# Kernel tuning notes

Hardware: AMD Instinct MI355X
Metric: run time of the kernel (lower is better)

## Reference

```python
import jax, jax.numpy as jnp
import numpy as np

K = 9          # neighbors
DIL = 1        # dilation
BN_EPS = 1e-5

def _bn(x, g, b, m, v):
    # inference batchnorm over channel (last) dim
    return (x - m) * (g * jax.lax.rsqrt(v + BN_EPS)) + b

def setup_inputs() -> dict:
    key = jax.random.key(0)
    ks = jax.random.split(key, 4)
    B, C, H, W = 8, 192, 56, 56
    Ch = 384
    s = 0.02
    return {
        'x': jax.random.normal(ks[0], (B, C, H, W), jnp.float32),
        'fc1_w': jax.random.normal(ks[1], (C, C), jnp.float32) * s,
        'fc1_b': jnp.zeros((C,), jnp.float32),
        'bn1_g': jnp.ones((C,), jnp.float32), 'bn1_b': jnp.zeros((C,), jnp.float32),
        'bn1_m': jnp.zeros((C,), jnp.float32), 'bn1_v': jnp.ones((C,), jnp.float32),
        'gc_w': jax.random.normal(ks[2], (Ch, 2 * C), jnp.float32) * s,
        'gc_b': jnp.zeros((Ch,), jnp.float32),
        'bn2_g': jnp.ones((Ch,), jnp.float32), 'bn2_b': jnp.zeros((Ch,), jnp.float32),
        'bn2_m': jnp.zeros((Ch,), jnp.float32), 'bn2_v': jnp.ones((Ch,), jnp.float32),
        'fc2_w': jax.random.normal(ks[3], (C, Ch), jnp.float32) * s,
        'fc2_b': jnp.zeros((C,), jnp.float32),
        'bn3_g': jnp.ones((C,), jnp.float32), 'bn3_b': jnp.zeros((C,), jnp.float32),
        'bn3_m': jnp.zeros((C,), jnp.float32), 'bn3_v': jnp.ones((C,), jnp.float32),
    }

def reference(x, fc1_w, fc1_b, bn1_g, bn1_b, bn1_m, bn1_v,
              gc_w, gc_b, bn2_g, bn2_b, bn2_m, bn2_v,
              fc2_w, fc2_b, bn3_g, bn3_b, bn3_m, bn3_v):
    B, C, H, W = x.shape
    N = H * W
    xf = x.reshape(B, C, N).transpose(0, 2, 1)          # (B, N, C) nodes
    shortcut = xf
    # fc1: 1x1 conv + BN
    h = _bn(jnp.einsum('bnc,oc->bno', xf, fc1_w) + fc1_b, bn1_g, bn1_b, bn1_m, bn1_v)
    # dynamic KNN on L2-normalized features (ViG dense_knn_matrix)
    hn = h / jnp.maximum(jnp.linalg.norm(h, axis=-1, keepdims=True), 1e-12)
    sim = jnp.einsum('bnc,bmc->bnm', hn, hn)            # (B, N, N) cosine sim
    _, idx = jax.lax.top_k(sim, K * DIL)                # nearest (incl. self)
    idx = idx[..., ::DIL]                               # dilated neighbors (B,N,K)
    # gather neighbor features
    x_j = jax.vmap(lambda hb, ib: hb[ib])(h, idx)       # (B, N, K, C)
    x_i = h[:, :, None, :]                              # (B, N, 1, C)
    feat = jnp.concatenate([jnp.broadcast_to(x_i, x_j.shape), x_j - x_i], axis=-1)
    # EdgeConv: conv then max over neighbors
    e = jnp.einsum('bnke,oe->bnko', feat, gc_w) + gc_b  # (B, N, K, Ch)
    m = jnp.max(e, axis=2)                              # (B, N, Ch)
    m = jax.nn.gelu(_bn(m, bn2_g, bn2_b, bn2_m, bn2_v), approximate=False)
    # fc2: 1x1 conv + BN, residual
    out = _bn(jnp.einsum('bnh,oh->bno', m, fc2_w) + fc2_b, bn3_g, bn3_b, bn3_m, bn3_v)
    out = out + shortcut
    return out.transpose(0, 2, 1).reshape(B, C, H, W)
```

## Files before the change

kernel.cpp:

```cpp
#include <hip/hip_runtime.h>

#define BDIM 256
#define NB 8
#define NC 192
#define NN 3136
#define NCH 384
#define NK 9
#define NROW (NB * NN)

typedef __attribute__((ext_vector_type(8))) short short8;
typedef __attribute__((ext_vector_type(4))) float f32x4;

__device__ __forceinline__ unsigned short f2bf(float f) {
  union { float f; unsigned u; } x{f};
  unsigned r = x.u + 0x7fff + ((x.u >> 16) & 1);
  return (unsigned short)(r >> 16);
}

__device__ __forceinline__ float bf2f(unsigned u16) {
  union { unsigned u; float f; } x{u16 << 16};
  return x.f;
}

__device__ __forceinline__ unsigned umax_(unsigned a, unsigned b) { return a > b ? a : b; }
__device__ __forceinline__ unsigned umin_(unsigned a, unsigned b) { return a < b ? a : b; }
#define UMAX3(a, b, c) umax_(umax_((a), (b)), (c))
#define CXD(x, y)                      \
  {                                    \
    unsigned h_ = umax_(x, y);         \
    unsigned l_ = umin_(x, y);         \
    x = h_;                            \
    y = l_;                            \
  }

__device__ __forceinline__ unsigned simkey(float f, unsigned it) {
  union { float f; unsigned u; } x{f + 2.0f};
  return (x.u & 0xFFFFF000u) | it;
}

__device__ __forceinline__ void gload16(const char* g, char* l) {
  __builtin_amdgcn_global_load_lds(
      (const __attribute__((address_space(1))) unsigned int*)g,
      (__attribute__((address_space(3))) unsigned int*)l, 16, 0, 0);
}

__device__ __forceinline__ void stage_tile(const char* gbase, char* lbuf, int t) {
#pragma unroll
  for (int i = 0; i < 6; ++i) {
    int L = (i * 256 + t) * 16;
    int m = L / 384;
    int kb = L - m * 384;
    gload16(gbase + m * 384 + (kb ^ ((m & 7) << 4)), lbuf + L);
  }
}

__global__ __launch_bounds__(BDIM) void k0_convw(
    const float* __restrict__ gw, const float* __restrict__ f1w,
    const float* __restrict__ f2w, unsigned short* __restrict__ gcwb,
    unsigned short* __restrict__ fc1b, unsigned short* __restrict__ fc2b) {
  int i = (blockIdx.x * BDIM + threadIdx.x) * 4;
  const float* src;
  unsigned short* dst;
  if (i < 147456) {
    int o = i / NC, k = i - o * NC;
    src = gw + (size_t)(o < NCH ? o : o - NCH) * (2 * NC) + (o < NCH ? 0 : NC) + k;
    dst = gcwb + i;
  } else if (i < 184320) {
    int j = i - 147456;
    src = f1w + j;
    dst = fc1b + j;
  } else {
    int j = i - 184320;
    int o = j / NCH, k = j - o * NCH;
    int oc = o >> 6, om = o & 63;
    int kh = k / 192, km = k - kh * 192;
    src = f2w + j;
    dst = fc2b + ((size_t)((oc * 2 + kh) * 64 + om)) * 192 + km;
  }
  float4 v = *(const float4*)src;
  uint2 u;
  u.x = (unsigned)f2bf(v.x) | ((unsigned)f2bf(v.y) << 16);
  u.y = (unsigned)f2bf(v.z) | ((unsigned)f2bf(v.w) << 16);
  *(uint2*)dst = u;
}

__global__ __launch_bounds__(384) void k0b_params(
    const float* __restrict__ f1b, const float* __restrict__ g1,
    const float* __restrict__ b1, const float* __restrict__ m1,
    const float* __restrict__ v1, const float* __restrict__ gcb,
    const float* __restrict__ g2, const float* __restrict__ b2,
    const float* __restrict__ m2, const float* __restrict__ v2,
    const float* __restrict__ f2b, const float* __restrict__ g3,
    const float* __restrict__ b3, const float* __restrict__ m3,
    const float* __restrict__ v3, float* __restrict__ sc1,
    float* __restrict__ sh1, float* __restrict__ sc2, float* __restrict__ sh2,
    float* __restrict__ sc3, float* __restrict__ sh3) {
  int c = threadIdx.x;
  if (c < NC) {
    float s1 = g1[c] * rsqrtf(v1[c] + 1e-5f);
    sc1[c] = s1;
    sh1[c] = (f1b[c] - m1[c]) * s1 + b1[c];
    float s3 = g3[c] * rsqrtf(v3[c] + 1e-5f);
    sc3[c] = s3;
    sh3[c] = (f2b[c] - m3[c]) * s3 + b3[c];
  }
  float s2 = g2[c] * rsqrtf(v2[c] + 1e-5f);
  sc2[c] = s2;
  sh2[c] = (gcb[c] - m2[c]) * s2 + b2[c];
}

__global__ __launch_bounds__(BDIM) void k1_mfma(
    const float* __restrict__ x, const unsigned short* __restrict__ fc1b,
    const float* __restrict__ sc1, const float* __restrict__ sh1,
    unsigned short* __restrict__ hnb, float* __restrict__ normo) {
  __shared__ __align__(16) char abuf[2][24576];
  int t = threadIdx.x;
  int b = blockIdx.x / 49, n0 = (blockIdx.x % 49) * 64;
  int lane = t & 63, w = t >> 6;
  int l15 = lane & 15, l4 = lane >> 4;
  int n = n0 + w * 16 + l15;
  short8 bfr[6];
  {
    const float* xcol = x + (size_t)b * NC * NN + n;
#pragma unroll
    for (int ks = 0; ks < 6; ++ks) {
      union { short8 s; unsigned u[4]; } pk;
#pragma unroll
      for (int j = 0; j < 4; ++j) {
        float v0 = xcol[(size_t)(ks * 32 + l4 * 8 + 2 * j) * NN];
        float v1 = xcol[(size_t)(ks * 32 + l4 * 8 + 2 * j + 1) * NN];
        pk.u[j] = (unsigned)f2bf(v0) | ((unsigned)f2bf(v1) << 16);
      }
      bfr[ks] = pk.s;
    }
  }
  f32x4 acc[3][4];
#pragma unroll
  for (int oc = 0; oc < 3; ++oc)
#pragma unroll
    for (int sub = 0; sub < 4; ++sub) acc[oc][sub] = {0.f, 0.f, 0.f, 0.f};

  const char* wB = (const char*)fc1b;
  stage_tile(wB, abuf[0], t);
  __syncthreads();
  for (int oc = 0; oc < 3; ++oc) {
    int cur = oc & 1;
    if (oc < 2) stage_tile(wB + (size_t)(oc + 1) * 24576, abuf[cur ^ 1], t);
#pragma unroll
    for (int sub = 0; sub < 4; ++sub) {
      int r_ = sub * 16 + l15;
      int rbase = r_ * 384, sw = (r_ & 7) << 4;
#pragma unroll
      for (int ks = 0; ks < 6; ++ks) {
        short8 af = *(const short8*)&abuf[cur][rbase + ((ks * 64 + l4 * 16) ^ sw)];
        acc[oc][sub] = __builtin_amdgcn_mfma_f32_16x16x32_bf16(af, bfr[ks],
                                                               acc[oc][sub], 0, 0, 0);
      }
    }
    __syncthreads();
  }
  float p = 0.f;
#pragma unroll
  for (int oc = 0; oc < 3; ++oc)
#pragma unroll
    for (int sub = 0; sub < 4; ++sub) {
      int c4 = oc * 64 + sub * 16 + l4 * 4;
      float s_[4], h_[4];
      *(float4*)s_ = *(const float4*)&sc1[c4];
      *(float4*)h_ = *(const float4*)&sh1[c4];
#pragma unroll
      for (int r = 0; r < 4; ++r) {
        float v = acc[oc][sub][r] * s_[r] + h_[r];
        acc[oc][sub][r] = v;
        p += v * v;
      }
    }
  p += __shfl_xor(p, 16);
  p += __shfl_xor(p, 32);
  float nr = fmaxf(sqrtf(p), 1e-12f);
  float iv = 1.f / nr;
  if (l4 == 0) normo[(size_t)b * NN + n] = nr;
#pragma unroll
  for (int oc = 0; oc < 3; ++oc)
#pragma unroll
    for (int sub = 0; sub < 4; ++sub) {
      uint2 u;
      u.x = (unsigned)f2bf(acc[oc][sub][0] * iv) |
            ((unsigned)f2bf(acc[oc][sub][1] * iv) << 16);
      u.y = (unsigned)f2bf(acc[oc][sub][2] * iv) |
            ((unsigned)f2bf(acc[oc][sub][3] * iv) << 16);
      *(uint2*)&hnb[(size_t)(b * NN + n) * NC + oc * 64 + sub * 16 + l4 * 4] = u;
    }
}

__global__ __launch_bounds__(512) void k23_fused(
    const unsigned short* __restrict__ hnb, const float* __restrict__ norm,
    const unsigned short* __restrict__ gcwb, unsigned* __restrict__ candK,
    unsigned short* __restrict__ P, unsigned short* __restrict__ Q) {
  __shared__ __align__(16) char abuf[2][12288];
  int t = threadIdx.x;
  int bid = blockIdx.x;
  int b = bid & 7;
  int j = bid >> 3;
  int lane = t & 63, w = t >> 6;
  int l15 = lane & 15, l4 = lane >> 4;
  int wg = w & 3, sub = w >> 2;
  const unsigned short* hb = hnb + (size_t)b * NN * NC;

  int LA = t * 16;
  int mA = LA / 384, kbA = LA - mA * 384;
  int gA = mA * 384 + (kbA ^ ((mA & 7) << 4));
  int LB = (384 + t) * 16;
  int mB = LB / 384, kbB = LB - mB * 384;
  int gB = mB * 384 + (kbB ^ ((mB & 7) << 4));
  bool stg = (t < 384);
  int r_ = sub * 16 + l15;
  int rbase = r_ * 384, sw = (r_ & 7) << 4;
  int dso[6];
#pragma unroll
  for (int ks = 0; ks < 6; ++ks) dso[ks] = rbase + ((ks * 64 + l4 * 16) ^ sw);

  if (j % 5 != 4) {
    int idx2a = (j / 5) * 4 + (j % 5);
    int n0 = (idx2a >> 2) * 64;
    int seg = idx2a & 3;
    int mt0 = (98 * seg) / 4, mt1 = (98 * (seg + 1)) / 4;
    const char* hbB = (const char*)hb;

    short8 bfr[6];
    {
      const short8* brow =
          (const short8*)(hb + (size_t)(n0 + wg * 16 + l15) * NC + l4 * 8);
#pragma unroll
      for (int ks = 0; ks < 6; ++ks) bfr[ks] = brow[ks * 4];
    }
    unsigned tk[NK];
#pragma unroll
    for (int r = 0; r < NK; ++r) tk[r] = 0u;

    {
      const char* src = hbB + (size_t)mt0 * 12288;
      if (stg) { gload16(src + gA, abuf[0] + LA); gload16(src + gB, abuf[0] + LB); }
    }
    __syncthreads();
    int nt = mt1 - mt0;
    for (int ti = 0; ti < nt; ++ti) {
      int cur = ti & 1;
      if (ti + 1 < nt) {
        const char* src = hbB + (size_t)(mt0 + ti + 1) * 12288;
        char* dl = abuf[cur ^ 1];
        if (stg) { gload16(src + gA, dl + LA); gload16(src + gB, dl + LB); }
        asm volatile("s_waitcnt vmcnt(2)" ::: "memory");
      } else {
        asm volatile("s_waitcnt vmcnt(0)" ::: "memory");
      }
      __builtin_amdgcn_s_barrier();
      __builtin_amdgcn_sched_barrier(0);
      const char* lb = abuf[cur];
      short8 af[6];
#pragma unroll
      for (int ks = 0; ks < 6; ++ks) af[ks] = *(const short8*)&lb[dso[ks]];
      f32x4 acc = {0.f, 0.f, 0.f, 0.f};
#pragma unroll
      for (int ks = 0; ks < 6; ++ks)
        acc = __builtin_amdgcn_mfma_f32_16x16x32_bf16(af[ks], bfr[ks], acc, 0, 0, 0);
      unsigned mknd = (unsigned)(4095 - ((mt0 + ti) * 32 + sub * 16 + l4 * 4));
      unsigned c0 = simkey(acc[0], mknd);
      unsigned c1 = simkey(acc[1], mknd - 1);
      unsigned c2 = simkey(acc[2], mknd - 2);
      unsigned c3 = simkey(acc[3], mknd - 3);
      CXD(c0, c1); CXD(c2, c3); CXD(c0, c2); CXD(c1, c3); CXD(c1, c2);
      tk[8] = UMAX3(UMAX3(tk[8], umin_(tk[7], c0), umin_(tk[6], c1)),
                    umin_(tk[5], c2), umin_(tk[4], c3));
      tk[7] = UMAX3(UMAX3(tk[7], umin_(tk[6], c0), umin_(tk[5], c1)),
                    umin_(tk[4], c2), umin_(tk[3], c3));
      tk[6] = UMAX3(UMAX3(tk[6], umin_(tk[5], c0), umin_(tk[4], c1)),
                    umin_(tk[3], c2), umin_(tk[2], c3));
      tk[5] = UMAX3(UMAX3(tk[5], umin_(tk[4], c0), umin_(tk[3], c1)),
                    umin_(tk[2], c2), umin_(tk[1], c3));
      tk[4] = UMAX3(UMAX3(tk[4], umin_(tk[3], c0), umin_(tk[2], c1)),
                    umin_(tk[1], c2), umin_(tk[0], c3));
      tk[3] = UMAX3(UMAX3(tk[3], c3, umin_(tk[2], c0)),
                    umin_(tk[1], c1), umin_(tk[0], c2));
      tk[2] = umax_(UMAX3(tk[2], c2, umin_(tk[1], c0)), umin_(tk[0], c1));
      tk[1] = UMAX3(tk[1], c1, umin_(tk[0], c0));
      tk[0] = umax_(tk[0], c0);
      __builtin_amdgcn_sched_barrier(0);
      __builtin_amdgcn_s_barrier();
    }
    unsigned* mkeys = (unsigned*)&abuf[0][0];
    int rw = wg * 16 + l15;
#pragma unroll
    for (int r = 0; r < NK; ++r) mkeys[(rw * 8 + sub * 4 + l4) * NK + r] = tk[r];
    __syncthreads();
    if (t < 256) {
      int row = t >> 2, g = t & 3;
      unsigned* a = &mkeys[(row * 8 + g) * NK];
      const unsigned* c = &mkeys[(row * 8 + g + 4) * NK];
      unsigned best[NK];
#pragma unroll
      for (int r = 0; r < NK; ++r) best[r] = 0u;
#pragma unroll
      for (int s = 0; s < 2 * NK; ++s) {
        unsigned cur_k = s < NK ? a[s] : c[s - NK];
#pragma unroll
        for (int q = 0; q < NK; ++q) {
          unsigned hi = best[q] > cur_k ? best[q] : cur_k;
          unsigned lo = best[q] > cur_k ? cur_k : best[q];
          best[q] = hi;
          cur_k = lo;
        }
      }
#pragma unroll
      for (int r = 0; r < NK; ++r) a[r] = best[r];
    }
    __syncthreads();
    if (t < 64) {
      const unsigned* src = &mkeys[(t * 8) * NK];
      unsigned best[NK];
#pragma unroll
      for (int r = 0; r < NK; ++r) best[r] = 0u;
      for (int s = 0; s < 36; ++s) {
        unsigned cur_k = src[s];
#pragma unroll
        for (int q = 0; q < NK; ++q) {
          unsigned hi = best[q] > cur_k ? best[q] : cur_k;
          unsigned lo = best[q] > cur_k ? cur_k : best[q];
          best[q] = hi;
          cur_k = lo;
        }
      }
      size_t row = (size_t)b * NN + n0 + t;
#pragma unroll
      for (int r = 0; r < NK; ++r)
        candK[(size_t)(seg * NK + r) * NROW + row] = best[r];
    }
  } else {
    int jj = j / 5;
    int n0 = jj * 64;
    int n = n0 + wg * 16 + l15;
    short8 bfr[6];
    {
      const short8* brow = (const short8*)(hb + (size_t)n * NC + l4 * 8);
#pragma unroll
      for (int ks = 0; ks < 6; ++ks) bfr[ks] = brow[ks * 4];
    }
    float nrm = norm[(size_t)b * NN + n];
    size_t orow = (size_t)b * NN + n;
    const char* wB = (const char*)gcwb;

    if (stg) { gload16(wB + gA, abuf[0] + LA); gload16(wB + gB, abuf[0] + LB); }
    __syncthreads();
    for (int ch = 0; ch < 24; ++ch) {
      int cur = ch & 1;
      if (ch < 23) {
        const char* src = wB + (size_t)(ch + 1) * 12288;
        char* dl = abuf[cur ^ 1];
        if (stg) { gload16(src + gA, dl + LA); gload16(src + gB, dl + LB); }
        asm volatile("s_waitcnt vmcnt(2)" ::: "memory");
      } else {
        asm volatile("s_waitcnt vmcnt(0)" ::: "memory");
      }
      __builtin_amdgcn_s_barrier();
      __builtin_amdgcn_sched_barrier(0);
      const char* lb = abuf[cur];
      f32x4 acc = {0.f, 0.f, 0.f, 0.f};
#pragma unroll
      for (int ks = 0; ks < 6; ++ks) {
        short8 af = *(const short8*)&lb[dso[ks]];
        acc = __builtin_amdgcn_mfma_f32_16x16x32_bf16(af, bfr[ks], acc, 0, 0, 0);
      }
      int o = ch * 32 + sub * 16 + l4 * 4;
      f32x4 st = acc * nrm;
      unsigned short* dst = (o < NCH) ? P : Q;
      int oo = (o < NCH) ? o : o - NCH;
      uint2 u;
      u.x = (unsigned)f2bf(st[0]) | ((unsigned)f2bf(st[1]) << 16);
      u.y = (unsigned)f2bf(st[2]) | ((unsigned)f2bf(st[3]) << 16);
      *(uint2*)&dst[orow * NCH + oo] = u;
      __builtin_amdgcn_sched_barrier(0);
      __builtin_amdgcn_s_barrier();
    }
  }
}

__global__ __launch_bounds__(BDIM) void k2b_merge(const unsigned* __restrict__ candK,
                                                  int* __restrict__ idxo) {
  int row = blockIdx.x * BDIM + threadIdx.x;
  unsigned tk[NK];
#pragma unroll
  for (int r = 0; r < NK; ++r) tk[r] = 0u;
  for (int s = 0; s < 4 * NK; ++s) {
    unsigned cur = candK[(size_t)s * NROW + row];
#pragma unroll
    for (int j = 0; j < NK; ++j) {
      unsigned hi = tk[j] > cur ? tk[j] : cur;
      unsigned lo = tk[j] > cur ? cur : tk[j];
      tk[j] = hi;
      cur = lo;
    }
  }
#pragma unroll
  for (int r = 0; r < NK; ++r)
    idxo[(size_t)row * NK + r] = 4095 - (int)(tk[r] & 4095u);
}

__global__ __launch_bounds__(BDIM) void k4_gathermax(
    const unsigned short* __restrict__ P, const unsigned short* __restrict__ Q,
    const int* __restrict__ idx, const float* __restrict__ sc2,
    const float* __restrict__ sh2, unsigned short* __restrict__ mbh) {
  int t = threadIdx.x;
  int lane = t & 63, wv = t >> 6;
  int b = blockIdx.x & 7;
  int n = (int)(blockIdx.x >> 3) * 4 + wv;
  size_t row = (size_t)b * NN + n;
  const int* ip = idx + row * NK;
  int id[NK];
#pragma unroll
  for (int k = 0; k < NK; ++k) id[k] = ip[k];
  const unsigned short* Qb = Q + (size_t)b * NN * NCH;
  const unsigned short* Pr = P + row * NCH;
  const unsigned short* Qr = Qb + (size_t)n * NCH;
#pragma unroll
  for (int j = 0; j < 3; ++j) {
    int o = j * 128 + lane * 2;
    float mx0 = -1e30f, mx1 = -1e30f;
#pragma unroll
    for (int k = 0; k < NK; ++k) {
      unsigned g = *(const unsigned*)&Qb[(size_t)id[k] * NCH + o];
      mx0 = fmaxf(mx0, bf2f(g & 0xffffu));
      mx1 = fmaxf(mx1, bf2f(g >> 16));
    }
    unsigned pv = *(const unsigned*)&Pr[o];
    unsigned qv = *(const unsigned*)&Qr[o];
    float2 ss = *(const float2*)&sc2[o];
    float2 hh = *(const float2*)&sh2[o];
    float e0 = bf2f(pv & 0xffffu) - bf2f(qv & 0xffffu) + mx0;
    float e1 = bf2f(pv >> 16) - bf2f(qv >> 16) + mx1;
    float y0 = e0 * ss.x + hh.x;
    float y1 = e1 * ss.y + hh.y;
    float ge0 = 0.5f * y0 * (1.f + erff(y0 * 0.70710678118654752f));
    float ge1 = 0.5f * y1 * (1.f + erff(y1 * 0.70710678118654752f));
    *(unsigned*)&mbh[row * NCH + o] =
        (unsigned)f2bf(ge0) | ((unsigned)f2bf(ge1) << 16);
  }
}

__global__ __launch_bounds__(BDIM) void k5_mfma(
    const unsigned short* __restrict__ mbh, const unsigned short* __restrict__ fc2b,
    const float* __restrict__ sc3, const float* __restrict__ sh3,
    const float* __restrict__ x, float* __restrict__ out) {
  __shared__ __align__(16) char abuf[2][24576];
  int t = threadIdx.x;
  int bid = blockIdx.x;
  int b = bid / 147;
  int rem = bid % 147;
  int n0 = (rem / 3) * 64;
  int oc = rem % 3;
  int lane = t & 63, w = t >> 6;
  int l15 = lane & 15, l4 = lane >> 4;
  int n = n0 + w * 16 + l15;
  short8 bfr[12];
  {
    const short8* brow = (const short8*)(mbh + (size_t)(b * NN + n) * NCH + l4 * 8);
#pragma unroll
    for (int kh = 0; kh < 2; ++kh)
#pragma unroll
      for (int ks = 0; ks < 6; ++ks) bfr[kh * 6 + ks] = brow[kh * 24 + ks * 4];
  }
  f32x4 acc[4];
#pragma unroll
  for (int sub = 0; sub < 4; ++sub) acc[sub] = {0.f, 0.f, 0.f, 0.f};

  const char* wt = (const char*)fc2b + (size_t)oc * 2 * 24576;
  stage_tile(wt, abuf[0], t);
  __syncthreads();
  for (int kh = 0; kh < 2; ++kh) {
    if (kh == 0) stage_tile(wt + 24576, abuf[1], t);
#pragma unroll
    for (int sub = 0; sub < 4; ++sub) {
      int r_ = sub * 16 + l15;
      int rbase = r_ * 384, sw = (r_ & 7) << 4;
#pragma unroll
      for (int ks = 0; ks < 6; ++ks) {
        short8 af = *(const short8*)&abuf[kh][rbase + ((ks * 64 + l4 * 16) ^ sw)];
        acc[sub] = __builtin_amdgcn_mfma_f32_16x16x32_bf16(af, bfr[kh * 6 + ks],
                                                           acc[sub], 0, 0, 0);
      }
    }
    __syncthreads();
  }
  const float* xb_ = x + (size_t)b * NC * NN;
  float* ob = out + (size_t)b * NC * NN;
#pragma unroll
  for (int sub = 0; sub < 4; ++sub) {
    int c4 = oc * 64 + sub * 16 + l4 * 4;
    float s_[4], h_[4];
    *(float4*)s_ = *(const float4*)&sc3[c4];
    *(float4*)h_ = *(const float4*)&sh3[c4];
#pragma unroll
    for (int r = 0; r < 4; ++r) {
      size_t off = (size_t)(c4 + r) * NN + n;
      ob[off] = acc[sub][r] * s_[r] + h_[r] + xb_[off];
    }
  }
}

extern "C" void kernel_launch(void* const* d_in, const int* in_sizes, int n_in,
                              void* d_out, int out_size, void* d_ws, size_t ws_size,
                              hipStream_t stream) {
  const float* x = (const float*)d_in[0];
  const float* fc1_w = (const float*)d_in[1];
  const float* fc1_b = (const float*)d_in[2];
  const float* bn1_g = (const float*)d_in[3];
  const float* bn1_b = (const float*)d_in[4];
  const float* bn1_m = (const float*)d_in[5];
  const float* bn1_v = (const float*)d_in[6];
  const float* gc_w = (const float*)d_in[7];
  const float* gc_b = (const float*)d_in[8];
  const float* bn2_g = (const float*)d_in[9];
  const float* bn2_b = (const float*)d_in[10];
  const float* bn2_m = (const float*)d_in[11];
  const float* bn2_v = (const float*)d_in[12];
  const float* fc2_w = (const float*)d_in[13];
  const float* fc2_b = (const float*)d_in[14];
  const float* bn3_g = (const float*)d_in[15];
  const float* bn3_b = (const float*)d_in[16];
  const float* bn3_m = (const float*)d_in[17];
  const float* bn3_v = (const float*)d_in[18];

  size_t nrow = (size_t)NROW;
  size_t npq = (size_t)NB * NN * NCH;
  size_t nhb = (size_t)NB * NN * NC;
  unsigned short* Pb = (unsigned short*)d_ws;
  unsigned short* Qb = Pb + npq;
  unsigned short* mbh = Qb + npq;
  float* norm = (float*)(mbh + npq);
  int* idx = (int*)(norm + nrow);
  unsigned short* hnb = (unsigned short*)(idx + nrow * NK);
  unsigned short* gcwb = hnb + nhb;
  unsigned short* fc1b = gcwb + 768 * NC;
  unsigned short* fc2b = fc1b + NC * NC;
  unsigned* candK = (unsigned*)(fc2b + NC * NCH);
  float* sc1 = (float*)(candK + 4 * NK * nrow);
  float* sh1 = sc1 + NC;
  float* sc2 = sh1 + NC;
  float* sh2 = sc2 + NCH;
  float* sc3 = sh2 + NCH;
  float* sh3 = sc3 + NC;

  k0_convw<<<252, BDIM, 0, stream>>>(gc_w, fc1_w, fc2_w, gcwb, fc1b, fc2b);
  k0b_params<<<1, 384, 0, stream>>>(fc1_b, bn1_g, bn1_b, bn1_m, bn1_v, gc_b,
                                    bn2_g, bn2_b, bn2_m, bn2_v, fc2_b, bn3_g,
                                    bn3_b, bn3_m, bn3_v, sc1, sh1, sc2, sh2,
                                    sc3, sh3);
  k1_mfma<<<NB * 49, BDIM, 0, stream>>>(x, fc1b, sc1, sh1, hnb, norm);
  k23_fused<<<NB * 245, 512, 0, stream>>>(hnb, norm, gcwb, candK, Pb, Qb);
  k2b_merge<<<NROW / BDIM, BDIM, 0, stream>>>(candK, idx);
  k4_gathermax<<<(NB * NN) / 4, BDIM, 0, stream>>>(Pb, Qb, idx, sc2, sh2, mbh);
  k5_mfma<<<NB * 147, BDIM, 0, stream>>>(mbh, fc2b, sc3, sh3, x, (float*)d_out);
}
```

Before: 146.9 us.

## Switch KNN similarity to 32x32 MFMA with larger tiles and 256-thread blocks

The fused similarity/top-k kernel now uses 256-thread blocks, each wave computing a 32x32 tile with mfma_f32_32x32x16_bf16 over 64-row candidate tiles staged through stage_tile into larger 24KB double buffers. This halves the number of tile iterations and removes the intermediate two-stage LDS merge of per-lane top-k lists, since each node now has only four partial lists. The projection branch is also reworked to 4 waves, each doing four 16-row subtiles per 64-row weight chunk. The cost is more registers (16 accumulators, 12 B fragments) and fewer threads per block, which may lower occupancy.

```diff
diff --git a/kernel.cpp b/kernel.cpp
--- a/kernel.cpp
+++ b/kernel.cpp
@@ -10,6 +10,7 @@
 
 typedef __attribute__((ext_vector_type(8))) short short8;
 typedef __attribute__((ext_vector_type(4))) float f32x4;
+typedef __attribute__((ext_vector_type(16))) float f32x16;
 
 __device__ __forceinline__ unsigned short f2bf(float f) {
   union { float f; unsigned u; } x{f};
@@ -31,6 +32,25 @@
     unsigned l_ = umin_(x, y);         \
     x = h_;                            \
     y = l_;                            \
+  }
+#define SEL94(c0, c1, c2, c3)                                              \
+  {                                                                        \
+    CXD(c0, c1); CXD(c2, c3); CXD(c0, c2); CXD(c1, c3); CXD(c1, c2);       \
+    tk[8] = UMAX3(UMAX3(tk[8], umin_(tk[7], c0), umin_(tk[6], c1)),        \
+                  umin_(tk[5], c2), umin_(tk[4], c3));                     \
+    tk[7] = UMAX3(UMAX3(tk[7], umin_(tk[6], c0), umin_(tk[5], c1)),        \
+                  umin_(tk[4], c2), umin_(tk[3], c3));                     \
+    tk[6] = UMAX3(UMAX3(tk[6], umin_(tk[5], c0), umin_(tk[4], c1)),        \
+                  umin_(tk[3], c2), umin_(tk[2], c3));                     \
+    tk[5] = UMAX3(UMAX3(tk[5], umin_(tk[4], c0), umin_(tk[3], c1)),        \
+                  umin_(tk[2], c2), umin_(tk[1], c3));                     \
+    tk[4] = UMAX3(UMAX3(tk[4], umin_(tk[3], c0), umin_(tk[2], c1)),        \
+                  umin_(tk[1], c2), umin_(tk[0], c3));                     \
+    tk[3] = UMAX3(UMAX3(tk[3], c3, umin_(tk[2], c0)),                      \
+                  umin_(tk[1], c1), umin_(tk[0], c2));                     \
+    tk[2] = umax_(UMAX3(tk[2], c2, umin_(tk[1], c0)), umin_(tk[0], c1));   \
+    tk[1] = UMAX3(tk[1], c1, umin_(tk[0], c0));                            \
+    tk[0] = umax_(tk[0], c0);                                              \
   }
 
 __device__ __forceinline__ unsigned simkey(float f, unsigned it) {
@@ -193,130 +213,84 @@
     }
 }
 
-__global__ __launch_bounds__(512) void k23_fused(
+__global__ __launch_bounds__(BDIM) void k23_fused(
     const unsigned short* __restrict__ hnb, const float* __restrict__ norm,
     const unsigned short* __restrict__ gcwb, unsigned* __restrict__ candK,
     unsigned short* __restrict__ P, unsigned short* __restrict__ Q) {
-  __shared__ __align__(16) char abuf[2][12288];
+  __shared__ __align__(16) char abuf[2][24576];
   int t = threadIdx.x;
   int bid = blockIdx.x;
   int b = bid & 7;
   int j = bid >> 3;
   int lane = t & 63, w = t >> 6;
-  int l15 = lane & 15, l4 = lane >> 4;
-  int wg = w & 3, sub = w >> 2;
   const unsigned short* hb = hnb + (size_t)b * NN * NC;
-
-  int LA = t * 16;
-  int mA = LA / 384, kbA = LA - mA * 384;
-  int gA = mA * 384 + (kbA ^ ((mA & 7) << 4));
-  int LB = (384 + t) * 16;
-  int mB = LB / 384, kbB = LB - mB * 384;
-  int gB = mB * 384 + (kbB ^ ((mB & 7) << 4));
-  bool stg = (t < 384);
-  int r_ = sub * 16 + l15;
-  int rbase = r_ * 384, sw = (r_ & 7) << 4;
-  int dso[6];
-#pragma unroll
-  for (int ks = 0; ks < 6; ++ks) dso[ks] = rbase + ((ks * 64 + l4 * 16) ^ sw);
 
   if (j % 5 != 4) {
     int idx2a = (j / 5) * 4 + (j % 5);
     int n0 = (idx2a >> 2) * 64;
     int seg = idx2a & 3;
-    int mt0 = (98 * seg) / 4, mt1 = (98 * (seg + 1)) / 4;
+    int mt0 = (49 * seg) / 4, mt1 = (49 * (seg + 1)) / 4;
     const char* hbB = (const char*)hb;
-
-    short8 bfr[6];
+    int l31 = lane & 31, hi = lane >> 5;
+    int nh = w & 1, mh = w >> 1;
+
+    short8 bfr[12];
     {
       const short8* brow =
-          (const short8*)(hb + (size_t)(n0 + wg * 16 + l15) * NC + l4 * 8);
-#pragma unroll
-      for (int ks = 0; ks < 6; ++ks) bfr[ks] = brow[ks * 4];
-    }
+          (const short8*)(hb + (size_t)(n0 + nh * 32 + l31) * NC + hi * 8);
+#pragma unroll
+      for (int ks = 0; ks < 12; ++ks) bfr[ks] = brow[ks * 2];
+    }
+    int row = mh * 32 + l31;
+    int rbase = row * 384, sw = (row & 7) << 4;
+    int dso[12];
+#pragma unroll
+    for (int ks = 0; ks < 12; ++ks) dso[ks] = rbase + ((ks * 32 + hi * 16) ^ sw);
+
     unsigned tk[NK];
 #pragma unroll
     for (int r = 0; r < NK; ++r) tk[r] = 0u;
 
-    {
-      const char* src = hbB + (size_t)mt0 * 12288;
-      if (stg) { gload16(src + gA, abuf[0] + LA); gload16(src + gB, abuf[0] + LB); }
-    }
-    __syncthreads();
+    stage_tile(hbB + (size_t)mt0 * 24576, abuf[0], t);
     int nt = mt1 - mt0;
+    int cur = 0;
     for (int ti = 0; ti < nt; ++ti) {
-      int cur = ti & 1;
       if (ti + 1 < nt) {
-        const char* src = hbB + (size_t)(mt0 + ti + 1) * 12288;
-        char* dl = abuf[cur ^ 1];
-        if (stg) { gload16(src + gA, dl + LA); gload16(src + gB, dl + LB); }
-        asm volatile("s_waitcnt vmcnt(2)" ::: "memory");
+        stage_tile(hbB + (size_t)(mt0 + ti + 1) * 24576, abuf[cur ^ 1], t);
+        asm volatile("s_waitcnt vmcnt(6)" ::: "memory");
       } else {
         asm volatile("s_waitcnt vmcnt(0)" ::: "memory");
       }
       __builtin_amdgcn_s_barrier();
       __builtin_amdgcn_sched_barrier(0);
       const char* lb = abuf[cur];
-      short8 af[6];
-#pragma unroll
-      for (int ks = 0; ks < 6; ++ks) af[ks] = *(const short8*)&lb[dso[ks]];
-      f32x4 acc = {0.f, 0.f, 0.f, 0.f};
-#pragma unroll
-      for (int ks = 0; ks < 6; ++ks)
-        acc = __builtin_amdgcn_mfma_f32_16x16x32_bf16(af[ks], bfr[ks], acc, 0, 0, 0);
-      unsigned mknd = (unsigned)(4095 - ((mt0 + ti) * 32 + sub * 16 + l4 * 4));
-      unsigned c0 = simkey(acc[0], mknd);
-      unsigned c1 = simkey(acc[1], mknd - 1);
-      unsigned c2 = simkey(acc[2], mknd - 2);
-      unsigned c3 = simkey(acc[3], mknd - 3);
-      CXD(c0, c1); CXD(c2, c3); CXD(c0, c2); CXD(c1, c3); CXD(c1, c2);
-      tk[8] = UMAX3(UMAX3(tk[8], umin_(tk[7], c0), umin_(tk[6], c1)),
-                    umin_(tk[5], c2), umin_(tk[4], c3));
-      tk[7] = UMAX3(UMAX3(tk[7], umin_(tk[6], c0), umin_(tk[5], c1)),
-                    umin_(tk[4], c2), umin_(tk[3], c3));
-      tk[6] = UMAX3(UMAX3(tk[6], umin_(tk[5], c0), umin_(tk[4], c1)),
-                    umin_(tk[3], c2), umin_(tk[2], c3));
-      tk[5] = UMAX3(UMAX3(tk[5], umin_(tk[4], c0), umin_(tk[3], c1)),
-                    umin_(tk[2], c2), umin_(tk[1], c3));
-      tk[4] = UMAX3(UMAX3(tk[4], umin_(tk[3], c0), umin_(tk[2], c1)),
-                    umin_(tk[1], c2), umin_(tk[0], c3));
-      tk[3] = UMAX3(UMAX3(tk[3], c3, umin_(tk[2], c0)),
-                    umin_(tk[1], c1), umin_(tk[0], c2));
-      tk[2] = umax_(UMAX3(tk[2], c2, umin_(tk[1], c0)), umin_(tk[0], c1));
-      tk[1] = UMAX3(tk[1], c1, umin_(tk[0], c0));
-      tk[0] = umax_(tk[0], c0);
+      f32x16 acc{};
+#pragma unroll
+      for (int ks = 0; ks < 12; ++ks) {
+        short8 af = *(const short8*)&lb[dso[ks]];
+        acc = __builtin_amdgcn_mfma_f32_32x32x16_bf16(af, bfr[ks], acc, 0, 0, 0);
+      }
+      unsigned mkb = (unsigned)(4095 - ((mt0 + ti) * 64 + mh * 32 + 4 * hi));
+#pragma unroll
+      for (int g = 0; g < 4; ++g) {
+        unsigned mkg = mkb - g * 8;
+        unsigned c0 = simkey(acc[4 * g + 0], mkg);
+        unsigned c1 = simkey(acc[4 * g + 1], mkg - 1);
+        unsigned c2 = simkey(acc[4 * g + 2], mkg - 2);
+        unsigned c3 = simkey(acc[4 * g + 3], mkg - 3);
+        SEL94(c0, c1, c2, c3);
+      }
       __builtin_amdgcn_sched_barrier(0);
       __builtin_amdgcn_s_barrier();
+      cur ^= 1;
     }
     unsigned* mkeys = (unsigned*)&abuf[0][0];
-    int rw = wg * 16 + l15;
-#pragma unroll
-    for (int r = 0; r < NK; ++r) mkeys[(rw * 8 + sub * 4 + l4) * NK + r] = tk[r];
-    __syncthreads();
-    if (t < 256) {
-      int row = t >> 2, g = t & 3;
-      unsigned* a = &mkeys[(row * 8 + g) * NK];
-      const unsigned* c = &mkeys[(row * 8 + g + 4) * NK];
-      unsigned best[NK];
-#pragma unroll
-      for (int r = 0; r < NK; ++r) best[r] = 0u;
-#pragma unroll
-      for (int s = 0; s < 2 * NK; ++s) {
-        unsigned cur_k = s < NK ? a[s] : c[s - NK];
-#pragma unroll
-        for (int q = 0; q < NK; ++q) {
-          unsigned hi = best[q] > cur_k ? best[q] : cur_k;
-          unsigned lo = best[q] > cur_k ? cur_k : best[q];
-          best[q] = hi;
-          cur_k = lo;
-        }
-      }
-#pragma unroll
-      for (int r = 0; r < NK; ++r) a[r] = best[r];
-    }
+    int slot = ((nh * 32 + l31) * 4 + mh * 2 + hi) * NK;
+#pragma unroll
+    for (int r = 0; r < NK; ++r) mkeys[slot + r] = tk[r];
     __syncthreads();
     if (t < 64) {
-      const unsigned* src = &mkeys[(t * 8) * NK];
+      const unsigned* src = &mkeys[t * 4 * NK];
       unsigned best[NK];
 #pragma unroll
       for (int r = 0; r < NK; ++r) best[r] = 0u;
@@ -324,21 +298,22 @@
         unsigned cur_k = src[s];
 #pragma unroll
         for (int q = 0; q < NK; ++q) {
-          unsigned hi = best[q] > cur_k ? best[q] : cur_k;
-          unsigned lo = best[q] > cur_k ? cur_k : best[q];
-          best[q] = hi;
-          cur_k = lo;
+          unsigned hi_ = best[q] > cur_k ? best[q] : cur_k;
+          unsigned lo_ = best[q] > cur_k ? cur_k : best[q];
+          best[q] = hi_;
+          cur_k = lo_;
         }
       }
-      size_t row = (size_t)b * NN + n0 + t;
+      size_t rowg = (size_t)b * NN + n0 + t;
 #pragma unroll
       for (int r = 0; r < NK; ++r)
-        candK[(size_t)(seg * NK + r) * NROW + row] = best[r];
+        candK[(size_t)(seg * NK + r) * NROW + rowg] = best[r];
     }
   } else {
     int jj = j / 5;
     int n0 = jj * 64;
-    int n = n0 + wg * 16 + l15;
+    int l15 = lane & 15, l4 = lane >> 4;
+    int n = n0 + w * 16 + l15;
     short8 bfr[6];
     {
       const short8* brow = (const short8*)(hb + (size_t)n * NC + l4 * 8);
@@ -349,37 +324,40 @@
     size_t orow = (size_t)b * NN + n;
     const char* wB = (const char*)gcwb;
 
-    if (stg) { gload16(wB + gA, abuf[0] + LA); gload16(wB + gB, abuf[0] + LB); }
-    __syncthreads();
-    for (int ch = 0; ch < 24; ++ch) {
-      int cur = ch & 1;
-      if (ch < 23) {
-        const char* src = wB + (size_t)(ch + 1) * 12288;
-        char* dl = abuf[cur ^ 1];
-        if (stg) { gload16(src + gA, dl + LA); gload16(src + gB, dl + LB); }
-        asm volatile("s_waitcnt vmcnt(2)" ::: "memory");
+    stage_tile(wB, abuf[0], t);
+    int cur = 0;
+    for (int ch = 0; ch < 12; ++ch) {
+      if (ch < 11) {
+        stage_tile(wB + (size_t)(ch + 1) * 24576, abuf[cur ^ 1], t);
+        asm volatile("s_waitcnt vmcnt(6)" ::: "memory");
       } else {
         asm volatile("s_waitcnt vmcnt(0)" ::: "memory");
       }
       __builtin_amdgcn_s_barrier();
       __builtin_amdgcn_sched_barrier(0);
       const char* lb = abuf[cur];
-      f32x4 acc = {0.f, 0.f, 0.f, 0.f};
-#pragma unroll
-      for (int ks = 0; ks < 6; ++ks) {
-        short8 af = *(const short8*)&lb[dso[ks]];
-        acc = __builtin_amdgcn_mfma_f32_16x16x32_bf16(af, bfr[ks], acc, 0, 0, 0);
-      }
-      int o = ch * 32 + sub * 16 + l4 * 4;
-      f32x4 st = acc * nrm;
-      unsigned short* dst = (o < NCH) ? P : Q;
-      int oo = (o < NCH) ? o : o - NCH;
-      uint2 u;
-      u.x = (unsigned)f2bf(st[0]) | ((unsigned)f2bf(st[1]) << 16);
-      u.y = (unsigned)f2bf(st[2]) | ((unsigned)f2bf(st[3]) << 16);
-      *(uint2*)&dst[orow * NCH + oo] = u;
+#pragma unroll
+      for (int sub = 0; sub < 4; ++sub) {
+        int mrow = sub * 16 + l15;
+        int rbase = mrow * 384, sw = (mrow & 7) << 4;
+        f32x4 acc = {0.f, 0.f, 0.f, 0.f};
+#pragma unroll
+        for (int ks = 0; ks < 6; ++ks) {
+          short8 af = *(const short8*)&lb[rbase + ((ks * 64 + l4 * 16) ^ sw)];
+          acc = __builtin_amdgcn_mfma_f32_16x16x32_bf16(af, bfr[ks], acc, 0, 0, 0);
+        }
+        int o = ch * 64 + sub * 16 + l4 * 4;
+        f32x4 st = acc * nrm;
+        unsigned short* dst = (o < NCH) ? P : Q;
+        int oo = (o < NCH) ? o : o - NCH;
+        uint2 u;
+        u.x = (unsigned)f2bf(st[0]) | ((unsigned)f2bf(st[1]) << 16);
+        u.y = (unsigned)f2bf(st[2]) | ((unsigned)f2bf(st[3]) << 16);
+        *(uint2*)&dst[orow * NCH + oo] = u;
+      }
       __builtin_amdgcn_sched_barrier(0);
       __builtin_amdgcn_s_barrier();
+      cur ^= 1;
     }
   }
 }
@@ -555,7 +533,7 @@
                                     bn3_b, bn3_m, bn3_v, sc1, sh1, sc2, sh2,
                                     sc3, sh3);
   k1_mfma<<<NB * 49, BDIM, 0, stream>>>(x, fc1b, sc1, sh1, hnb, norm);
-  k23_fused<<<NB * 245, 512, 0, stream>>>(hnb, norm, gcwb, candK, Pb, Qb);
+  k23_fused<<<NB * 245, BDIM, 0, stream>>>(hnb, norm, gcwb, candK, Pb, Qb);
   k2b_merge<<<NROW / BDIM, BDIM, 0, stream>>>(candK, idx);
   k4_gathermax<<<(NB * NN) / 4, BDIM, 0, stream>>>(Pb, Qb, idx, sc2, sh2, mbh);
   k5_mfma<<<NB * 147, BDIM, 0, stream>>>(mbh, fc2b, sc3, sh3, x, (float*)d_out);
```

After: 145.0 us. Within noise of the previous version (-1.3%).
